# Kernel optimization log

Hardware: AMD Instinct MI355X
Metric: run time of the kernel (lower is better)

The kernel has to match this reference:

```python
import jax, jax.numpy as jnp
import numpy as np

N = 50000       # nodes (atoms)
E = 1600000     # edges (avg degree 32)
NAB = 128       # n_atom_basis
NF = 128        # n_filters
NG = 50         # n_gaussians
CUTOFF = 5.0


def ssp(x):
    # shifted softplus: softplus(x) - log(2)
    return jax.nn.softplus(x) - jnp.log(2.0).astype(x.dtype)


def setup_inputs() -> dict:
    key = jax.random.key(0)
    ks = jax.random.split(key, 12)
    r = jax.random.normal(ks[0], (N, NAB), dtype=jnp.float32)
    e = jax.random.uniform(ks[1], (E, 1), dtype=jnp.float32) * CUTOFF
    a = jax.random.randint(ks[2], (E, 2), 0, N, dtype=jnp.int64)
    s = lambda k, shp, fan_in: jax.random.normal(k, shp, dtype=jnp.float32) / np.sqrt(fan_in)
    return {
        "r": r, "e": e, "a": a,
        "W_df1": s(ks[3], (NG, NG), NG),  "b_df1": jnp.zeros((NG,), jnp.float32),
        "W_df2": s(ks[4], (NG, NF), NG),  "b_df2": jnp.zeros((NF,), jnp.float32),
        "W_af":  s(ks[5], (NAB, NF), NAB),
        "W_d1":  s(ks[6], (NF, NAB), NF), "b_d1": jnp.zeros((NAB,), jnp.float32),
        "W_d2":  s(ks[7], (NAB, NAB), NAB), "b_d2": jnp.zeros((NAB,), jnp.float32),
    }


def reference(r, e, a, W_df1, b_df1, W_df2, b_df2, W_af, W_d1, b_d1, W_d2, b_d2):
    # Gaussian smearing of distances: [E,1] -> [E,NG]
    offset = jnp.linspace(0.0, CUTOFF, NG, dtype=r.dtype)
    width = offset[1] - offset[0]
    coeff = -0.5 / (width * width)
    g = jnp.exp(coeff * (e - offset) ** 2)            # [E, NG]
    # distance filter MLP
    ef = ssp(g @ W_df1 + b_df1) @ W_df2 + b_df2       # [E, NF]
    # atom filter (no bias)
    rf = r @ W_af                                     # [N, NF]
    # gather-multiply messages
    src, dst = a[:, 0], a[:, 1]
    m1 = rf[src] * ef                                 # [E, NF]
    m2 = rf[dst] * ef                                 # [E, NF]
    # scatter-add aggregation (symmetric)
    agg = jax.ops.segment_sum(m1, dst, num_segments=N) + \
          jax.ops.segment_sum(m2, src, num_segments=N)  # [N, NF]
    # node update MLP
    out = ssp(agg @ W_d1 + b_d1) @ W_d2 + b_d2        # [N, NAB]
    return out
```

## Files before the change

### kernel.cpp

```cpp
#include <hip/hip_runtime.h>
#include <hip/hip_fp16.h>
#include <math.h>

#define NAB 128
#define NG 50
#define TK 1024
#define BN 128
#define CAPB 8704
#define NBLK 256
#define TPB 1024
#define NBMAX 400

__device__ __forceinline__ float sspf(float x) {
  float t = __expf(-fabsf(x));
  return fmaxf(x, 0.0f) + __logf(1.0f + t) - 0.69314718055994531f;
}

__global__ __launch_bounds__(128)
void gemm128(const float* __restrict__ A, const float* __restrict__ W,
             const float* __restrict__ bias, void* __restrict__ Cout,
             int M, int mode) {
  __shared__ float Al[32 * 128];
  const int tid = threadIdx.x;
  const int r0 = blockIdx.x * 32;
  const int rows = min(32, M - r0);

  {
    const float4* A4 = (const float4*)(A + (size_t)r0 * NAB);
    float4* Al4 = (float4*)Al;
    for (int f = tid; f < rows * 32; f += 128) Al4[f] = A4[f];
  }
  __syncthreads();

  const int c = tid & 31;
  const int gq = tid >> 5;
  float acc[8][4];
#pragma unroll
  for (int j = 0; j < 8; ++j) {
    acc[j][0] = 0.f; acc[j][1] = 0.f; acc[j][2] = 0.f; acc[j][3] = 0.f;
  }
  const float4* W4 = (const float4*)W;
  for (int i = 0; i < 128; i += 4) {
    float4 w0 = W4[(i + 0) * 32 + c];
    float4 w1 = W4[(i + 1) * 32 + c];
    float4 w2 = W4[(i + 2) * 32 + c];
    float4 w3 = W4[(i + 3) * 32 + c];
#pragma unroll
    for (int j = 0; j < 8; ++j) {
      float4 av = *(const float4*)&Al[(gq * 8 + j) * 128 + i];
      acc[j][0] += av.x * w0.x + av.y * w1.x + av.z * w2.x + av.w * w3.x;
      acc[j][1] += av.x * w0.y + av.y * w1.y + av.z * w2.y + av.w * w3.y;
      acc[j][2] += av.x * w0.z + av.y * w1.z + av.z * w2.z + av.w * w3.z;
      acc[j][3] += av.x * w0.w + av.y * w1.w + av.z * w2.w + av.w * w3.w;
    }
  }
  float4 bv = make_float4(0.f, 0.f, 0.f, 0.f);
  if (bias) bv = *(const float4*)&bias[4 * c];
#pragma unroll
  for (int j = 0; j < 8; ++j) {
    int row = gq * 8 + j;
    if (row < rows) {
      float4 o;
      o.x = acc[j][0] + bv.x;
      o.y = acc[j][1] + bv.y;
      o.z = acc[j][2] + bv.z;
      o.w = acc[j][3] + bv.w;
      if (mode == 1) { o.x = sspf(o.x); o.y = sspf(o.y); o.z = sspf(o.z); o.w = sspf(o.w); }
      if (mode == 2) {
        __half2 h01 = __floats2half2_rn(o.x, o.y);
        __half2 h23 = __floats2half2_rn(o.z, o.w);
        uint2 u;
        u.x = *(unsigned*)&h01;
        u.y = *(unsigned*)&h23;
        *(uint2*)((__half*)Cout + (size_t)(r0 + row) * NAB + 4 * c) = u;
      } else {
        *(float4*)((float*)Cout + (size_t)(r0 + row) * NAB + 4 * c) = o;
      }
    }
  }
}

__global__ __launch_bounds__(128)
void build_tp(const float* __restrict__ W1, const float* __restrict__ b1,
              const float* __restrict__ W2, const float* __restrict__ b2,
              uint2* __restrict__ Th) {
  __shared__ float h0[NG], h1[NG], e0[NAB], e1[NAB];
  const int k = blockIdx.x;
  const int tid = threadIdx.x;
  constexpr float width = 5.0f / 49.0f;
  constexpr float coeff = -0.5f / (width * width);
  const float x0 = (float)k * (5.0f / (float)(TK - 1));
  const float x1 = (float)(k + 1) * (5.0f / (float)(TK - 1));

  if (tid < NG) {
    float a0 = b1[tid], a1 = b1[tid];
    for (int i = 0; i < NG; ++i) {
      float w = W1[i * NG + tid];
      float d0 = x0 - i * width;
      float d1 = x1 - i * width;
      a0 = __fmaf_rn(__expf(coeff * d0 * d0), w, a0);
      a1 = __fmaf_rn(__expf(coeff * d1 * d1), w, a1);
    }
    h0[tid] = sspf(a0);
    h1[tid] = sspf(a1);
  }
  __syncthreads();
  float f0 = b2[tid], f1 = b2[tid];
#pragma unroll 10
  for (int i = 0; i < NG; ++i) {
    float w = W2[i * NAB + tid];
    f0 = __fmaf_rn(h0[i], w, f0);
    f1 = __fmaf_rn(h1[i], w, f1);
  }
  e0[tid] = f0;
  e1[tid] = f1;
  __syncthreads();
  if (tid < 64) {
    float b0 = e0[2 * tid],      d0 = e1[2 * tid]     - e0[2 * tid];
    float b1v = e0[2 * tid + 1], d1 = e1[2 * tid + 1] - e0[2 * tid + 1];
    __half2 p0 = __floats2half2_rn(b0, d0);
    __half2 p1 = __floats2half2_rn(b1v, d1);
    uint2 u;
    u.x = *(unsigned*)&p0;
    u.y = *(unsigned*)&p1;
    Th[(size_t)k * 64 + tid] = u;
  }
}

__global__ __launch_bounds__(TPB)
void hist_pass(const int2* __restrict__ a2, int* __restrict__ hist,
               int E, int NB) {
  __shared__ int h[NBMAX];
  const int blk = blockIdx.x;
  const int chunk = (E + NBLK - 1) / NBLK;
  const int lo = blk * chunk;
  const int hi = min(E, lo + chunk);
  for (int i = threadIdx.x; i < NB; i += TPB) h[i] = 0;
  __syncthreads();
  for (int i = lo + threadIdx.x; i < hi; i += TPB) {
    int2 p = a2[i];
    atomicAdd(&h[p.y >> 7], 1);
    atomicAdd(&h[p.x >> 7], 1);
  }
  __syncthreads();
  for (int i = threadIdx.x; i < NB; i += TPB) hist[i * NBLK + blk] = h[i];
}

__global__ __launch_bounds__(NBLK)
void scan_bucket(int* __restrict__ hist, int* __restrict__ btot) {
  __shared__ int s[NBLK];
  const int b = blockIdx.x;
  const int t = threadIdx.x;
  int v = hist[b * NBLK + t];
  s[t] = v;
  __syncthreads();
  for (int d = 1; d < NBLK; d <<= 1) {
    int u = (t >= d) ? s[t - d] : 0;
    __syncthreads();
    s[t] += u;
    __syncthreads();
  }
  hist[b * NBLK + t] = s[t] - v;
  if (t == NBLK - 1) btot[b] = s[t];
}

__global__ __launch_bounds__(512)
void scan_bbase(const int* __restrict__ btot, int* __restrict__ bbase, int NB) {
  __shared__ int s[512];
  int t = threadIdx.x;
  int v = (t < NB) ? btot[t] : 0;
  s[t] = v;
  __syncthreads();
  for (int d = 1; d < 512; d <<= 1) {
    int u = (t >= d) ? s[t - d] : 0;
    __syncthreads();
    s[t] += u;
    __syncthreads();
  }
  if (t < NB) bbase[t] = s[t] - v;
}

__global__ __launch_bounds__(TPB)
void scatter_pass(const int2* __restrict__ a2, const float* __restrict__ e,
                  const int* __restrict__ hist, const int* __restrict__ bbase,
                  int2* __restrict__ items, int E, int NB) {
  __shared__ int cur[NBMAX];
  const int blk = blockIdx.x;
  const int chunk = (E + NBLK - 1) / NBLK;
  const int lo = blk * chunk;
  const int hi = min(E, lo + chunk);
  for (int i = threadIdx.x; i < NB; i += TPB)
    cur[i] = bbase[i] + hist[i * NBLK + blk];
  __syncthreads();
  const float scale = (float)(TK - 1) / 5.0f;
  for (int i = lo + threadIdx.x; i < hi; i += TPB) {
    int2 p = a2[i];
    float x = e[i] * scale;
    int k = min((int)x, TK - 2);
    float f = x - (float)k;
    int payload = (k << 16) | (int)__half_as_ushort(__float2half_rn(f));
    int pos0 = atomicAdd(&cur[p.y >> 7], 1);
    items[pos0] = make_int2(p.x | ((p.y & 127) << 16), payload);
    int pos1 = atomicAdd(&cur[p.x >> 7], 1);
    items[pos1] = make_int2(p.y | ((p.x & 127) << 16), payload);
  }
}

__global__ __launch_bounds__(256)
void local_sort(const int* __restrict__ bbase, const int* __restrict__ btot,
                int2* __restrict__ items,
                int* __restrict__ nstart, int* __restrict__ nend, int N) {
  __shared__ int2 lit[CAPB];
  __shared__ int bin[BN], cur[BN], scn[BN];
  const int b = blockIdx.x;
  const int tid = threadIdx.x;
  const int cnt = min(btot[b], CAPB);
  const int base = bbase[b];

  for (int i = tid; i < cnt; i += 256) lit[i] = items[base + i];
  if (tid < BN) bin[tid] = 0;
  __syncthreads();
  for (int i = tid; i < cnt; i += 256) atomicAdd(&bin[(lit[i].x >> 16) & (BN - 1)], 1);
  __syncthreads();
  if (tid < BN) scn[tid] = bin[tid];
  __syncthreads();
  for (int d = 1; d < BN; d <<= 1) {
    int v = 0;
    if (tid < BN && tid >= d) v = scn[tid - d];
    __syncthreads();
    if (tid < BN) scn[tid] += v;
    __syncthreads();
  }
  if (tid < BN) {
    int incl = scn[tid];
    int excl = incl - bin[tid];
    cur[tid] = excl;
    int n = b * BN + tid;
    if (n < N) {
      nstart[n] = base + excl;
      nend[n]   = base + incl;
    }
  }
  __syncthreads();
  for (int i = tid; i < cnt; i += 256) {
    int2 it = lit[i];
    int pos = atomicAdd(&cur[(it.x >> 16) & (BN - 1)], 1);
    items[base + pos] = it;
  }
}

__global__ __launch_bounds__(256)
void pull_kernel(const int* __restrict__ nstart, const int* __restrict__ nend,
                 const int2* __restrict__ items, const __half* __restrict__ rfh,
                 const uint2* __restrict__ Th, float* __restrict__ agg, int N) {
  const int wv = __builtin_amdgcn_readfirstlane(threadIdx.x >> 6);
  const int n = blockIdx.x * 4 + wv;
  if (n >= N) return;
  const int l = threadIdx.x & 63;
  int j  = nstart[n];
  const int j1 = nend[n];
  float a0 = 0.f, a1 = 0.f;

  for (; j + 4 <= j1; j += 4) {
    int2 p0 = items[j + 0];
    int2 p1 = items[j + 1];
    int2 p2 = items[j + 2];
    int2 p3 = items[j + 3];
    int sx0 = __builtin_amdgcn_readfirstlane(p0.x);
    int sy0 = __builtin_amdgcn_readfirstlane(p0.y);
    int sx1 = __builtin_amdgcn_readfirstlane(p1.x);
    int sy1 = __builtin_amdgcn_readfirstlane(p1.y);
    int sx2 = __builtin_amdgcn_readfirstlane(p2.x);
    int sy2 = __builtin_amdgcn_readfirstlane(p2.y);
    int sx3 = __builtin_amdgcn_readfirstlane(p3.x);
    int sy3 = __builtin_amdgcn_readfirstlane(p3.y);
    const uint2* tp0 = Th + ((size_t)(sy0 >> 16) << 6);
    const uint2* tp1 = Th + ((size_t)(sy1 >> 16) << 6);
    const uint2* tp2 = Th + ((size_t)(sy2 >> 16) << 6);
    const uint2* tp3 = Th + ((size_t)(sy3 >> 16) << 6);
    const __half* rp0 = rfh + ((size_t)(sx0 & 0xffff) << 7);
    const __half* rp1 = rfh + ((size_t)(sx1 & 0xffff) << 7);
    const __half* rp2 = rfh + ((size_t)(sx2 & 0xffff) << 7);
    const __half* rp3 = rfh + ((size_t)(sx3 & 0xffff) << 7);
    uint2 t0 = tp0[l];
    uint2 t1 = tp1[l];
    uint2 t2 = tp2[l];
    uint2 t3 = tp3[l];
    unsigned q0 = *(const unsigned*)(rp0 + 2 * l);
    unsigned q1 = *(const unsigned*)(rp1 + 2 * l);
    unsigned q2 = *(const unsigned*)(rp2 + 2 * l);
    unsigned q3 = *(const unsigned*)(rp3 + 2 * l);
    float f0 = __half2float(__ushort_as_half((unsigned short)sy0));
    float f1 = __half2float(__ushort_as_half((unsigned short)sy1));
    float f2 = __half2float(__ushort_as_half((unsigned short)sy2));
    float f3 = __half2float(__ushort_as_half((unsigned short)sy3));
    float2 r0 = __half22float2(*(const __half2*)&q0);
    float2 r1 = __half22float2(*(const __half2*)&q1);
    float2 r2 = __half22float2(*(const __half2*)&q2);
    float2 r3 = __half22float2(*(const __half2*)&q3);
    {
      float2 b0 = __half22float2(*(const __half2*)&t0.x);
      float2 c0 = __half22float2(*(const __half2*)&t0.y);
      a0 = __fmaf_rn(r0.x, __fmaf_rn(f0, b0.y, b0.x), a0);
      a1 = __fmaf_rn(r0.y, __fmaf_rn(f0, c0.y, c0.x), a1);
    }
    {
      float2 b1 = __half22float2(*(const __half2*)&t1.x);
      float2 c1 = __half22float2(*(const __half2*)&t1.y);
      a0 = __fmaf_rn(r1.x, __fmaf_rn(f1, b1.y, b1.x), a0);
      a1 = __fmaf_rn(r1.y, __fmaf_rn(f1, c1.y, c1.x), a1);
    }
    {
      float2 b2 = __half22float2(*(const __half2*)&t2.x);
      float2 c2 = __half22float2(*(const __half2*)&t2.y);
      a0 = __fmaf_rn(r2.x, __fmaf_rn(f2, b2.y, b2.x), a0);
      a1 = __fmaf_rn(r2.y, __fmaf_rn(f2, c2.y, c2.x), a1);
    }
    {
      float2 b3 = __half22float2(*(const __half2*)&t3.x);
      float2 c3 = __half22float2(*(const __half2*)&t3.y);
      a0 = __fmaf_rn(r3.x, __fmaf_rn(f3, b3.y, b3.x), a0);
      a1 = __fmaf_rn(r3.y, __fmaf_rn(f3, c3.y, c3.x), a1);
    }
  }
  for (; j < j1; ++j) {
    int2 p = items[j];
    int sx = __builtin_amdgcn_readfirstlane(p.x);
    int sy = __builtin_amdgcn_readfirstlane(p.y);
    const uint2* tp = Th + ((size_t)(sy >> 16) << 6);
    const __half* rp = rfh + ((size_t)(sx & 0xffff) << 7);
    uint2 tv = tp[l];
    unsigned qq = *(const unsigned*)(rp + 2 * l);
    float fr = __half2float(__ushort_as_half((unsigned short)sy));
    float2 rv = __half22float2(*(const __half2*)&qq);
    float2 bb = __half22float2(*(const __half2*)&tv.x);
    float2 cc = __half22float2(*(const __half2*)&tv.y);
    a0 = __fmaf_rn(rv.x, __fmaf_rn(fr, bb.y, bb.x), a0);
    a1 = __fmaf_rn(rv.y, __fmaf_rn(fr, cc.y, cc.x), a1);
  }
  float2 o; o.x = a0; o.y = a1;
  *(float2*)&agg[((size_t)n << 7) + 2 * l] = o;
}

extern "C" void kernel_launch(void* const* d_in, const int* in_sizes, int n_in,
                              void* d_out, int out_size, void* d_ws, size_t ws_size,
                              hipStream_t stream) {
  const float* r     = (const float*)d_in[0];
  const float* e     = (const float*)d_in[1];
  const int*   a     = (const int*)d_in[2];
  const float* W_df1 = (const float*)d_in[3];
  const float* b_df1 = (const float*)d_in[4];
  const float* W_df2 = (const float*)d_in[5];
  const float* b_df2 = (const float*)d_in[6];
  const float* W_af  = (const float*)d_in[7];
  const float* W_d1  = (const float*)d_in[8];
  const float* b_d1  = (const float*)d_in[9];
  const float* W_d2  = (const float*)d_in[10];
  const float* b_d2  = (const float*)d_in[11];

  const int N = in_sizes[0] / NAB;
  const int E = in_sizes[1];
  const int H = 2 * E;
  const int NB = (N + BN - 1) / BN;

  char* base = (char*)d_ws;
  size_t items_bytes = (size_t)H * sizeof(int2);
  size_t t1_bytes = (size_t)N * NAB * sizeof(float);
  size_t shared_bytes = items_bytes > t1_bytes ? items_bytes : t1_bytes;
  int2*   items  = (int2*)base;
  float*  t1     = (float*)base;
  float*  agg    = (float*)(base + shared_bytes);
  __half* rfh    = (__half*)(agg + (size_t)N * NAB);
  uint2*  Th     = (uint2*)(rfh + (size_t)N * NAB);
  int*    hist   = (int*)(Th + (size_t)(TK - 1) * 64);
  int*    btot   = hist + (size_t)NB * NBLK;
  int*    bbase  = btot + NB;
  int*    nstart = bbase + NB;
  int*    nend   = nstart + N;

  const int gblocks = (N + 31) / 32;

  build_tp<<<TK - 1, 128, 0, stream>>>(W_df1, b_df1, W_df2, b_df2, Th);
  gemm128<<<gblocks, 128, 0, stream>>>(r, W_af, nullptr, rfh, N, 2);
  hist_pass<<<NBLK, TPB, 0, stream>>>((const int2*)a, hist, E, NB);
  scan_bucket<<<NB, NBLK, 0, stream>>>(hist, btot);
  scan_bbase<<<1, 512, 0, stream>>>(btot, bbase, NB);
  scatter_pass<<<NBLK, TPB, 0, stream>>>((const int2*)a, e, hist, bbase, items, E, NB);
  local_sort<<<NB, 256, 0, stream>>>(bbase, btot, items, nstart, nend, N);
  pull_kernel<<<(N + 3) / 4, 256, 0, stream>>>(nstart, nend, items, rfh, Th, agg, N);
  gemm128<<<gblocks, 128, 0, stream>>>(agg, W_d1, b_d1, t1, N, 1);
  gemm128<<<gblocks, 128, 0, stream>>>(t1, W_d2, b_d2, d_out, N, 0);
}
```

Baseline: 404.5 us.

## Fuse node-update GEMMs and batch pull-kernel edge index loads with lane broadcast

The two node-update MLP GEMMs are merged into one kernel that keeps the ssp intermediate in shared memory, so the N x 128 fp32 intermediate no longer makes a round trip through global memory. The pull kernel now loads 8 edge items with one vector load spread across lanes, broadcasts them with readlane, and prefetches the next batch. This gives each wave 8 independent gathers in flight per iteration instead of 4. The fused GEMM doubles shared memory per block, which may lower occupancy, and the wider unroll adds register pressure.

```diff
diff --git a/kernel.cpp b/kernel.cpp
--- a/kernel.cpp
+++ b/kernel.cpp
@@ -81,6 +81,101 @@
 }
 
 __global__ __launch_bounds__(128)
+void gemm128x2(const float* __restrict__ A, const float* __restrict__ W1,
+               const float* __restrict__ b1, const float* __restrict__ W2,
+               const float* __restrict__ b2, float* __restrict__ out, int M) {
+  __shared__ float Al[32 * 128];
+  __shared__ float Tl[32 * 128];
+  const int tid = threadIdx.x;
+  const int r0 = blockIdx.x * 32;
+  const int rows = min(32, M - r0);
+
+  {
+    const float4* A4 = (const float4*)(A + (size_t)r0 * NAB);
+    float4* Al4 = (float4*)Al;
+    for (int f = tid; f < rows * 32; f += 128) Al4[f] = A4[f];
+  }
+  __syncthreads();
+
+  const int c = tid & 31;
+  const int gq = tid >> 5;
+  float acc[8][4];
+
+#pragma unroll
+  for (int j = 0; j < 8; ++j) {
+    acc[j][0] = 0.f; acc[j][1] = 0.f; acc[j][2] = 0.f; acc[j][3] = 0.f;
+  }
+  {
+    const float4* W4 = (const float4*)W1;
+    for (int i = 0; i < 128; i += 4) {
+      float4 w0 = W4[(i + 0) * 32 + c];
+      float4 w1 = W4[(i + 1) * 32 + c];
+      float4 w2 = W4[(i + 2) * 32 + c];
+      float4 w3 = W4[(i + 3) * 32 + c];
+#pragma unroll
+      for (int j = 0; j < 8; ++j) {
+        float4 av = *(const float4*)&Al[(gq * 8 + j) * 128 + i];
+        acc[j][0] += av.x * w0.x + av.y * w1.x + av.z * w2.x + av.w * w3.x;
+        acc[j][1] += av.x * w0.y + av.y * w1.y + av.z * w2.y + av.w * w3.y;
+        acc[j][2] += av.x * w0.z + av.y * w1.z + av.z * w2.z + av.w * w3.z;
+        acc[j][3] += av.x * w0.w + av.y * w1.w + av.z * w2.w + av.w * w3.w;
+      }
+    }
+  }
+  {
+    float4 bv = *(const float4*)&b1[4 * c];
+#pragma unroll
+    for (int j = 0; j < 8; ++j) {
+      int row = gq * 8 + j;
+      float4 o;
+      o.x = sspf(acc[j][0] + bv.x);
+      o.y = sspf(acc[j][1] + bv.y);
+      o.z = sspf(acc[j][2] + bv.z);
+      o.w = sspf(acc[j][3] + bv.w);
+      *(float4*)&Tl[row * 128 + 4 * c] = o;
+    }
+  }
+  __syncthreads();
+
+#pragma unroll
+  for (int j = 0; j < 8; ++j) {
+    acc[j][0] = 0.f; acc[j][1] = 0.f; acc[j][2] = 0.f; acc[j][3] = 0.f;
+  }
+  {
+    const float4* W4 = (const float4*)W2;
+    for (int i = 0; i < 128; i += 4) {
+      float4 w0 = W4[(i + 0) * 32 + c];
+      float4 w1 = W4[(i + 1) * 32 + c];
+      float4 w2 = W4[(i + 2) * 32 + c];
+      float4 w3 = W4[(i + 3) * 32 + c];
+#pragma unroll
+      for (int j = 0; j < 8; ++j) {
+        float4 av = *(const float4*)&Tl[(gq * 8 + j) * 128 + i];
+        acc[j][0] += av.x * w0.x + av.y * w1.x + av.z * w2.x + av.w * w3.x;
+        acc[j][1] += av.x * w0.y + av.y * w1.y + av.z * w2.y + av.w * w3.y;
+        acc[j][2] += av.x * w0.z + av.y * w1.z + av.z * w2.z + av.w * w3.z;
+        acc[j][3] += av.x * w0.w + av.y * w1.w + av.z * w2.w + av.w * w3.w;
+      }
+    }
+  }
+  {
+    float4 bv = *(const float4*)&b2[4 * c];
+#pragma unroll
+    for (int j = 0; j < 8; ++j) {
+      int row = gq * 8 + j;
+      if (row < rows) {
+        float4 o;
+        o.x = acc[j][0] + bv.x;
+        o.y = acc[j][1] + bv.y;
+        o.z = acc[j][2] + bv.z;
+        o.w = acc[j][3] + bv.w;
+        *(float4*)&out[(size_t)(r0 + row) * NAB + 4 * c] = o;
+      }
+    }
+  }
+}
+
+__global__ __launch_bounds__(128)
 void build_tp(const float* __restrict__ W1, const float* __restrict__ b1,
               const float* __restrict__ W2, const float* __restrict__ b2,
               uint2* __restrict__ Th) {
@@ -261,80 +356,47 @@
   const int j1 = nend[n];
   float a0 = 0.f, a1 = 0.f;
 
-  for (; j + 4 <= j1; j += 4) {
-    int2 p0 = items[j + 0];
-    int2 p1 = items[j + 1];
-    int2 p2 = items[j + 2];
-    int2 p3 = items[j + 3];
-    int sx0 = __builtin_amdgcn_readfirstlane(p0.x);
-    int sy0 = __builtin_amdgcn_readfirstlane(p0.y);
-    int sx1 = __builtin_amdgcn_readfirstlane(p1.x);
-    int sy1 = __builtin_amdgcn_readfirstlane(p1.y);
-    int sx2 = __builtin_amdgcn_readfirstlane(p2.x);
-    int sy2 = __builtin_amdgcn_readfirstlane(p2.y);
-    int sx3 = __builtin_amdgcn_readfirstlane(p3.x);
-    int sy3 = __builtin_amdgcn_readfirstlane(p3.y);
-    const uint2* tp0 = Th + ((size_t)(sy0 >> 16) << 6);
-    const uint2* tp1 = Th + ((size_t)(sy1 >> 16) << 6);
-    const uint2* tp2 = Th + ((size_t)(sy2 >> 16) << 6);
-    const uint2* tp3 = Th + ((size_t)(sy3 >> 16) << 6);
-    const __half* rp0 = rfh + ((size_t)(sx0 & 0xffff) << 7);
-    const __half* rp1 = rfh + ((size_t)(sx1 & 0xffff) << 7);
-    const __half* rp2 = rfh + ((size_t)(sx2 & 0xffff) << 7);
-    const __half* rp3 = rfh + ((size_t)(sx3 & 0xffff) << 7);
-    uint2 t0 = tp0[l];
-    uint2 t1 = tp1[l];
-    uint2 t2 = tp2[l];
-    uint2 t3 = tp3[l];
-    unsigned q0 = *(const unsigned*)(rp0 + 2 * l);
-    unsigned q1 = *(const unsigned*)(rp1 + 2 * l);
-    unsigned q2 = *(const unsigned*)(rp2 + 2 * l);
-    unsigned q3 = *(const unsigned*)(rp3 + 2 * l);
-    float f0 = __half2float(__ushort_as_half((unsigned short)sy0));
-    float f1 = __half2float(__ushort_as_half((unsigned short)sy1));
-    float f2 = __half2float(__ushort_as_half((unsigned short)sy2));
-    float f3 = __half2float(__ushort_as_half((unsigned short)sy3));
-    float2 r0 = __half22float2(*(const __half2*)&q0);
-    float2 r1 = __half22float2(*(const __half2*)&q1);
-    float2 r2 = __half22float2(*(const __half2*)&q2);
-    float2 r3 = __half22float2(*(const __half2*)&q3);
-    {
-      float2 b0 = __half22float2(*(const __half2*)&t0.x);
-      float2 c0 = __half22float2(*(const __half2*)&t0.y);
-      a0 = __fmaf_rn(r0.x, __fmaf_rn(f0, b0.y, b0.x), a0);
-      a1 = __fmaf_rn(r0.y, __fmaf_rn(f0, c0.y, c0.x), a1);
-    }
-    {
-      float2 b1 = __half22float2(*(const __half2*)&t1.x);
-      float2 c1 = __half22float2(*(const __half2*)&t1.y);
-      a0 = __fmaf_rn(r1.x, __fmaf_rn(f1, b1.y, b1.x), a0);
-      a1 = __fmaf_rn(r1.y, __fmaf_rn(f1, c1.y, c1.x), a1);
-    }
-    {
-      float2 b2 = __half22float2(*(const __half2*)&t2.x);
-      float2 c2 = __half22float2(*(const __half2*)&t2.y);
-      a0 = __fmaf_rn(r2.x, __fmaf_rn(f2, b2.y, b2.x), a0);
-      a1 = __fmaf_rn(r2.y, __fmaf_rn(f2, c2.y, c2.x), a1);
-    }
-    {
-      float2 b3 = __half22float2(*(const __half2*)&t3.x);
-      float2 c3 = __half22float2(*(const __half2*)&t3.y);
-      a0 = __fmaf_rn(r3.x, __fmaf_rn(f3, b3.y, b3.x), a0);
-      a1 = __fmaf_rn(r3.y, __fmaf_rn(f3, c3.y, c3.x), a1);
-    }
+  int2 cur;
+  if (j + 8 <= j1) cur = items[j + (l & 7)];
+  while (j + 8 <= j1) {
+    int sx[8], sy[8];
+#pragma unroll
+    for (int i = 0; i < 8; ++i) {
+      sx[i] = __builtin_amdgcn_readlane(cur.x, i);
+      sy[i] = __builtin_amdgcn_readlane(cur.y, i);
+    }
+    const int jn = j + 8;
+    if (jn + 8 <= j1) cur = items[jn + (l & 7)];
+    uint2 tv[8];
+    unsigned qv[8];
+#pragma unroll
+    for (int i = 0; i < 8; ++i) {
+      tv[i] = Th[(((size_t)((unsigned)sy[i] >> 16)) << 6) + l];
+      qv[i] = *(const unsigned*)(rfh + (((size_t)(sx[i] & 0xffff)) << 7) + 2 * l);
+    }
+#pragma unroll
+    for (int i = 0; i < 8; ++i) {
+      float f = __half2float(__ushort_as_half((unsigned short)(sy[i] & 0xffff)));
+      float2 rv = __half22float2(*(const __half2*)&qv[i]);
+      float2 bb = __half22float2(*(const __half2*)&tv[i].x);
+      float2 cc = __half22float2(*(const __half2*)&tv[i].y);
+      a0 = __fmaf_rn(rv.x, __fmaf_rn(f, bb.y, bb.x), a0);
+      a1 = __fmaf_rn(rv.y, __fmaf_rn(f, cc.y, cc.x), a1);
+    }
+    j = jn;
   }
   for (; j < j1; ++j) {
     int2 p = items[j];
     int sx = __builtin_amdgcn_readfirstlane(p.x);
     int sy = __builtin_amdgcn_readfirstlane(p.y);
-    const uint2* tp = Th + ((size_t)(sy >> 16) << 6);
+    const uint2* tp = Th + ((size_t)((unsigned)sy >> 16) << 6);
     const __half* rp = rfh + ((size_t)(sx & 0xffff) << 7);
-    uint2 tv = tp[l];
+    uint2 tvv = tp[l];
     unsigned qq = *(const unsigned*)(rp + 2 * l);
-    float fr = __half2float(__ushort_as_half((unsigned short)sy));
+    float fr = __half2float(__ushort_as_half((unsigned short)(sy & 0xffff)));
     float2 rv = __half22float2(*(const __half2*)&qq);
-    float2 bb = __half22float2(*(const __half2*)&tv.x);
-    float2 cc = __half22float2(*(const __half2*)&tv.y);
+    float2 bb = __half22float2(*(const __half2*)&tvv.x);
+    float2 cc = __half22float2(*(const __half2*)&tvv.y);
     a0 = __fmaf_rn(rv.x, __fmaf_rn(fr, bb.y, bb.x), a0);
     a1 = __fmaf_rn(rv.y, __fmaf_rn(fr, cc.y, cc.x), a1);
   }
@@ -364,12 +426,8 @@
   const int NB = (N + BN - 1) / BN;
 
   char* base = (char*)d_ws;
-  size_t items_bytes = (size_t)H * sizeof(int2);
-  size_t t1_bytes = (size_t)N * NAB * sizeof(float);
-  size_t shared_bytes = items_bytes > t1_bytes ? items_bytes : t1_bytes;
   int2*   items  = (int2*)base;
-  float*  t1     = (float*)base;
-  float*  agg    = (float*)(base + shared_bytes);
+  float*  agg    = (float*)(base + (size_t)H * sizeof(int2));
   __half* rfh    = (__half*)(agg + (size_t)N * NAB);
   uint2*  Th     = (uint2*)(rfh + (size_t)N * NAB);
   int*    hist   = (int*)(Th + (size_t)(TK - 1) * 64);
@@ -388,6 +446,5 @@
   scatter_pass<<<NBLK, TPB, 0, stream>>>((const int2*)a, e, hist, bbase, items, E, NB);
   local_sort<<<NB, 256, 0, stream>>>(bbase, btot, items, nstart, nend, N);
   pull_kernel<<<(N + 3) / 4, 256, 0, stream>>>(nstart, nend, items, rfh, Th, agg, N);
-  gemm128<<<gblocks, 128, 0, stream>>>(agg, W_d1, b_d1, t1, N, 1);
-  gemm128<<<gblocks, 128, 0, stream>>>(t1, W_d2, b_d2, d_out, N, 0);
-}
+  gemm128x2<<<gblocks, 128, 0, stream>>>(agg, W_d1, b_d1, W_d2, b_d2, (float*)d_out, N);
+}
```

Result: slower. 419.1 us (+3.6%).
